# Kernel optimization log

Hardware: AMD Instinct MI355X
Metric: run time of the kernel (lower is better)

The kernel has to match this reference:

```python
import jax, jax.numpy as jnp
import numpy as np

B, SQ, SK = 8, 128, 128
IVD, DIM, EV, H, NH = 32, 32, 64, 8, 128
DK = EV // H


def setup_inputs() -> dict:
    key = jax.random.key(0)
    ks = jax.random.split(key, 16)
    n = lambda k, s: jax.random.normal(k, s, dtype=jnp.float32)
    lin = lambda k, fi, fo: n(k, (fi, fo)) / np.float32(np.sqrt(fi))
    d = {}
    d['query_value'] = n(ks[0], (B, SQ, IVD))
    d['key_value']   = n(ks[1], (B, SK, IVD))
    d['value']       = n(ks[2], (B, SK, DIM))
    d['impute_data'] = n(ks[3], (B, SQ, IVD // 2))
    d['emb_mask'] = jax.random.randint(ks[4], (B, SK, DIM), 0, 2).astype(jnp.int32)
    # learn_value_embedding: Linear(IVD,NH)+Tanh+Linear(NH,EV,no bias)
    d['w1'] = lin(ks[5], IVD, NH); d['b1'] = jnp.zeros((NH,), jnp.float32)
    d['w2'] = lin(ks[6], NH, EV)
    # linears[0], linears[1]: Linear(EV,EV)
    d['wq'] = lin(ks[7], EV, EV); d['bq'] = jnp.zeros((EV,), jnp.float32)
    d['wk'] = lin(ks[8], EV, EV); d['bk'] = jnp.zeros((EV,), jnp.float32)
    # linears[2]: Linear(DIM*H, NH)
    d['wo'] = lin(ks[9], DIM * H, NH); d['bo'] = jnp.zeros((NH,), jnp.float32)
    # query_data_enc: Linear(IVD/2,NH)+LayerNorm(NH)+ReLU+Linear(NH,NH)
    d['wd1'] = lin(ks[10], IVD // 2, NH); d['bd1'] = jnp.zeros((NH,), jnp.float32)
    d['ln_g'] = jnp.ones((NH,), jnp.float32); d['ln_b'] = jnp.zeros((NH,), jnp.float32)
    d['wd2'] = lin(ks[11], NH, NH); d['bd2'] = jnp.zeros((NH,), jnp.float32)
    return d


def reference(query_value, key_value, value, impute_data,
              w1, b1, w2, wq, bq, wk, bk, wo, bo,
              wd1, bd1, ln_g, ln_b, wd2, bd2, emb_mask):
    b = query_value.shape[0]
    dim = value.shape[-1]
    # value embeddings: Linear -> Tanh -> Linear(no bias)
    qe = jnp.tanh(query_value @ w1 + b1) @ w2   # [B,Sq,EV]
    ke = jnp.tanh(key_value @ w1 + b1) @ w2     # [B,Sk,EV]
    q = (qe @ wq + bq).reshape(b, -1, H, DK).transpose(0, 2, 1, 3)  # [B,H,Sq,DK]
    k = (ke @ wk + bk).reshape(b, -1, H, DK).transpose(0, 2, 1, 3)  # [B,H,Sk,DK]
    scores = jnp.einsum('bhqd,bhkd->bhqk', q, k) / np.float32(np.sqrt(DK))
    # broadcast scores over the value channel dim; masked_fill with -10000
    m = emb_mask[:, None, None, :, :]           # [B,1,1,Sk,dim]
    logits = jnp.where(m == 0, jnp.float32(-10000.0), scores[..., None])  # [B,H,Sq,Sk,dim]
    p_attn = jax.nn.softmax(logits, axis=-2)    # softmax over Sk per channel
    out = jnp.einsum('bhqkd,bkd->bhqd', p_attn, value)  # [B,H,Sq,dim]
    x = out.transpose(0, 2, 1, 3).reshape(b, -1, H * dim)
    y = x @ wo + bo                             # [B,Sq,NH]
    # query_data_enc branch
    h1 = impute_data @ wd1 + bd1
    mu = jnp.mean(h1, axis=-1, keepdims=True)
    var = jnp.var(h1, axis=-1, keepdims=True)
    ln = (h1 - mu) / jnp.sqrt(var + 1e-5) * ln_g + ln_b
    query_data = jax.nn.relu(ln) @ wd2 + bd2    # [B,Sq,NH]
    return y, query_data
```

## Files before the change

### kernel.cpp

```cpp
#include <hip/hip_runtime.h>
#include <math.h>

#define B 8
#define SQ 128
#define SK 128
#define IVD 32
#define DIM 32
#define EV 64
#define H 8
#define NH 128
#define DK 8

__global__ __launch_bounds__(128) void proj_kernel(
    const float* __restrict__ qv, const float* __restrict__ kv,
    const float* __restrict__ w1, const float* __restrict__ b1,
    const float* __restrict__ w2,
    const float* __restrict__ wq, const float* __restrict__ bq,
    const float* __restrict__ wk, const float* __restrict__ bk,
    float* __restrict__ qout, float* __restrict__ kout)
{
    const int r = blockIdx.x;
    const int tid = threadIdx.x;
    const float* src; const float* wp; const float* bp; float* dst;
    if (r < B * SQ) {
        src = qv + r * IVD; wp = wq; bp = bq; dst = qout + r * EV;
    } else {
        int rr = r - B * SQ;
        src = kv + rr * IVD; wp = wk; bp = bk; dst = kout + rr * EV;
    }
    __shared__ float xs[IVD];
    __shared__ float h1[NH];
    __shared__ float ev[EV];
    if (tid < IVD) xs[tid] = src[tid];
    __syncthreads();
    float acc = b1[tid];
    #pragma unroll
    for (int i = 0; i < IVD; ++i) acc += xs[i] * w1[i * NH + tid];
    h1[tid] = tanhf(acc);
    __syncthreads();
    if (tid < EV) {
        float a = 0.f;
        #pragma unroll 8
        for (int i = 0; i < NH; ++i) a += h1[i] * w2[i * EV + tid];
        ev[tid] = a;
    }
    __syncthreads();
    if (tid < EV) {
        float a = bp[tid];
        #pragma unroll 8
        for (int j = 0; j < EV; ++j) a += ev[j] * wp[j * EV + tid];
        dst[tid] = a;
    }
}

__global__ __launch_bounds__(256) void attn_kernel(
    const float* __restrict__ qproj, const float* __restrict__ kproj,
    const float* __restrict__ value, const int* __restrict__ mask,
    const float* __restrict__ wo, const float* __restrict__ bo,
    float* __restrict__ y)
{
    const int bq = blockIdx.x;
    const int b = bq >> 7;
    const int tid = threadIdx.x;

    __shared__ float qs[EV];
    __shared__ float sc[H * SK];
    __shared__ float hmax[H];
    __shared__ float vm[SK * DIM];
    __shared__ float mm[SK * DIM];
    __shared__ float xr[H * DIM];
    __shared__ float ypart[256];

    if (tid < EV) qs[tid] = qproj[bq * EV + tid];
    for (int idx = tid; idx < SK * DIM; idx += 256) {
        vm[idx] = value[b * SK * DIM + idx];
        mm[idx] = (float)mask[b * SK * DIM + idx];
    }
    __syncthreads();

    for (int p = tid; p < H * SK; p += 256) {
        const int h = p >> 7, k = p & 127;
        const float* kr = kproj + (b * SK + k) * EV + h * DK;
        float d = 0.f;
        #pragma unroll
        for (int j = 0; j < DK; ++j) d += qs[h * DK + j] * kr[j];
        sc[p] = d * 0.3535533905932738f;
    }
    __syncthreads();

    if (tid < H) {
        float m = -1e30f;
        for (int k = 0; k < SK; ++k) m = fmaxf(m, sc[tid * SK + k]);
        hmax[tid] = m;
    }
    __syncthreads();
    for (int p = tid; p < H * SK; p += 256) {
        const int h = p >> 7;
        sc[p] = __expf(sc[p] - hmax[h]);
    }
    __syncthreads();

    {
        const int h = tid >> 5, d = tid & 31;
        float num = 0.f, den = 0.f;
        #pragma unroll 4
        for (int k = 0; k < SK; ++k) {
            const float w = sc[h * SK + k] * mm[k * DIM + d];
            num += w * vm[k * DIM + d];
            den += w;
        }
        xr[tid] = num / den;
    }
    __syncthreads();

    {
        const int n = tid & 127, half = tid >> 7;
        const float* wop = wo + half * 128 * NH;
        const float* xp = xr + half * 128;
        float a = 0.f;
        #pragma unroll 8
        for (int j = 0; j < 128; ++j) a += xp[j] * wop[j * NH + n];
        ypart[tid] = a;
    }
    __syncthreads();
    if (tid < NH) {
        y[bq * NH + tid] = ypart[tid] + ypart[tid + 128] + bo[tid];
    }
}

__global__ __launch_bounds__(128) void impute_kernel(
    const float* __restrict__ imp,
    const float* __restrict__ wd1, const float* __restrict__ bd1,
    const float* __restrict__ ln_g, const float* __restrict__ ln_b,
    const float* __restrict__ wd2, const float* __restrict__ bd2,
    float* __restrict__ out)
{
    const int bs = blockIdx.x;
    const int tid = threadIdx.x;
    __shared__ float xs[IVD / 2];
    __shared__ float h1[NH];
    __shared__ float red[2];

    if (tid < IVD / 2) xs[tid] = imp[bs * (IVD / 2) + tid];
    __syncthreads();
    float acc = bd1[tid];
    #pragma unroll
    for (int i = 0; i < IVD / 2; ++i) acc += xs[i] * wd1[i * NH + tid];

    float s = acc;
    #pragma unroll
    for (int off = 32; off > 0; off >>= 1) s += __shfl_down(s, off, 64);
    if ((tid & 63) == 0) red[tid >> 6] = s;
    __syncthreads();
    const float mean = (red[0] + red[1]) * (1.f / NH);
    const float diff = acc - mean;
    float s2 = diff * diff;
    __syncthreads();
    #pragma unroll
    for (int off = 32; off > 0; off >>= 1) s2 += __shfl_down(s2, off, 64);
    if ((tid & 63) == 0) red[tid >> 6] = s2;
    __syncthreads();
    const float var = (red[0] + red[1]) * (1.f / NH);

    const float ln = diff * rsqrtf(var + 1e-5f) * ln_g[tid] + ln_b[tid];
    h1[tid] = fmaxf(ln, 0.f);
    __syncthreads();

    float a = bd2[tid];
    #pragma unroll 8
    for (int j = 0; j < NH; ++j) a += h1[j] * wd2[j * NH + tid];
    out[bs * NH + tid] = a;
}

extern "C" void kernel_launch(void* const* d_in, const int* in_sizes, int n_in,
                              void* d_out, int out_size, void* d_ws, size_t ws_size,
                              hipStream_t stream) {
    const float* query_value = (const float*)d_in[0];
    const float* key_value   = (const float*)d_in[1];
    const float* value       = (const float*)d_in[2];
    const float* impute      = (const float*)d_in[3];
    const int*   emb_mask    = (const int*)d_in[4];
    const float* w1   = (const float*)d_in[5];
    const float* b1   = (const float*)d_in[6];
    const float* w2   = (const float*)d_in[7];
    const float* wq   = (const float*)d_in[8];
    const float* bq   = (const float*)d_in[9];
    const float* wk   = (const float*)d_in[10];
    const float* bk   = (const float*)d_in[11];
    const float* wo   = (const float*)d_in[12];
    const float* bo   = (const float*)d_in[13];
    const float* wd1  = (const float*)d_in[14];
    const float* bd1  = (const float*)d_in[15];
    const float* ln_g = (const float*)d_in[16];
    const float* ln_b = (const float*)d_in[17];
    const float* wd2  = (const float*)d_in[18];
    const float* bd2  = (const float*)d_in[19];

    float* y  = (float*)d_out;
    float* qd = y + B * SQ * NH;

    float* qproj = (float*)d_ws;
    float* kproj = qproj + B * SQ * EV;

    hipLaunchKernelGGL(proj_kernel, dim3(B * (SQ + SK)), dim3(128), 0, stream,
                       query_value, key_value, w1, b1, w2, wq, bq, wk, bk, qproj, kproj);
    hipLaunchKernelGGL(attn_kernel, dim3(B * SQ), dim3(256), 0, stream,
                       qproj, kproj, value, emb_mask, wo, bo, y);
    hipLaunchKernelGGL(impute_kernel, dim3(B * SQ), dim3(128), 0, stream,
                       impute, wd1, bd1, ln_g, ln_b, wd2, bd2, qd);
}
```

Before: 127.6 us.

## Fuse impute into projection kernel and process two queries per attention block

```diff
diff --git a/kernel.cpp b/kernel.cpp
--- a/kernel.cpp
+++ b/kernel.cpp
@@ -10,46 +10,100 @@
 #define H 8
 #define NH 128
 #define DK 8
-
-__global__ __launch_bounds__(128) void proj_kernel(
+#define TQ 2
+#define PAD 132
+
+__global__ __launch_bounds__(128) void fused1_kernel(
     const float* __restrict__ qv, const float* __restrict__ kv,
     const float* __restrict__ w1, const float* __restrict__ b1,
     const float* __restrict__ w2,
-    const float* __restrict__ wq, const float* __restrict__ bq,
-    const float* __restrict__ wk, const float* __restrict__ bk,
-    float* __restrict__ qout, float* __restrict__ kout)
+    const float* __restrict__ wq, const float* __restrict__ bqv,
+    const float* __restrict__ wk, const float* __restrict__ bkv,
+    float* __restrict__ qout, float* __restrict__ kout,
+    const float* __restrict__ imp,
+    const float* __restrict__ wd1, const float* __restrict__ bd1,
+    const float* __restrict__ ln_g, const float* __restrict__ ln_b,
+    const float* __restrict__ wd2, const float* __restrict__ bd2,
+    float* __restrict__ qd)
 {
     const int r = blockIdx.x;
     const int tid = threadIdx.x;
-    const float* src; const float* wp; const float* bp; float* dst;
-    if (r < B * SQ) {
-        src = qv + r * IVD; wp = wq; bp = bq; dst = qout + r * EV;
+
+    if (r < 2 * B * SQ) {
+        __shared__ float xs[IVD];
+        __shared__ float h1[NH];
+        __shared__ float ev[EV];
+        __shared__ float part[128];
+        const float* src; const float* wp; const float* bp; float* dst;
+        if (r < B * SQ) {
+            src = qv + r * IVD; wp = wq; bp = bqv; dst = qout + r * EV;
+        } else {
+            const int rr = r - B * SQ;
+            src = kv + rr * IVD; wp = wk; bp = bkv; dst = kout + rr * EV;
+        }
+        if (tid < IVD) xs[tid] = src[tid];
+        __syncthreads();
+        float acc = b1[tid];
+        #pragma unroll
+        for (int i = 0; i < IVD; ++i) acc += xs[i] * w1[i * NH + tid];
+        h1[tid] = tanhf(acc);
+        __syncthreads();
+
+        const int o = tid & 63, hf = tid >> 6;
+        {
+            float a = 0.f;
+            const float* w2p = w2 + o;
+            #pragma unroll 8
+            for (int i = hf * 64; i < hf * 64 + 64; ++i) a += h1[i] * w2p[i * EV];
+            part[tid] = a;
+        }
+        __syncthreads();
+        if (tid < EV) ev[tid] = part[tid] + part[tid + 64];
+        __syncthreads();
+        {
+            float a = 0.f;
+            const float* wpp = wp + o;
+            #pragma unroll 8
+            for (int j = hf * 32; j < hf * 32 + 32; ++j) a += ev[j] * wpp[j * EV];
+            part[tid] = a;
+        }
+        __syncthreads();
+        if (tid < EV) dst[tid] = part[tid] + part[tid + 64] + bp[tid];
     } else {
-        int rr = r - B * SQ;
-        src = kv + rr * IVD; wp = wk; bp = bk; dst = kout + rr * EV;
-    }
-    __shared__ float xs[IVD];
-    __shared__ float h1[NH];
-    __shared__ float ev[EV];
-    if (tid < IVD) xs[tid] = src[tid];
-    __syncthreads();
-    float acc = b1[tid];
-    #pragma unroll
-    for (int i = 0; i < IVD; ++i) acc += xs[i] * w1[i * NH + tid];
-    h1[tid] = tanhf(acc);
-    __syncthreads();
-    if (tid < EV) {
-        float a = 0.f;
+        const int bs = r - 2 * B * SQ;
+        __shared__ float xs2[IVD / 2];
+        __shared__ float h1b[NH];
+        __shared__ float red[2];
+
+        if (tid < IVD / 2) xs2[tid] = imp[bs * (IVD / 2) + tid];
+        __syncthreads();
+        float acc = bd1[tid];
+        #pragma unroll
+        for (int i = 0; i < IVD / 2; ++i) acc += xs2[i] * wd1[i * NH + tid];
+
+        float s = acc;
+        #pragma unroll
+        for (int off = 32; off > 0; off >>= 1) s += __shfl_down(s, off, 64);
+        if ((tid & 63) == 0) red[tid >> 6] = s;
+        __syncthreads();
+        const float mean = (red[0] + red[1]) * (1.f / NH);
+        const float diff = acc - mean;
+        float s2 = diff * diff;
+        __syncthreads();
+        #pragma unroll
+        for (int off = 32; off > 0; off >>= 1) s2 += __shfl_down(s2, off, 64);
+        if ((tid & 63) == 0) red[tid >> 6] = s2;
+        __syncthreads();
+        const float var = (red[0] + red[1]) * (1.f / NH);
+
+        const float ln = diff * rsqrtf(var + 1e-5f) * ln_g[tid] + ln_b[tid];
+        h1b[tid] = fmaxf(ln, 0.f);
+        __syncthreads();
+
+        float a = bd2[tid];
         #pragma unroll 8
-        for (int i = 0; i < NH; ++i) a += h1[i] * w2[i * EV + tid];
-        ev[tid] = a;
-    }
-    __syncthreads();
-    if (tid < EV) {
-        float a = bp[tid];
-        #pragma unroll 8
-        for (int j = 0; j < EV; ++j) a += ev[j] * wp[j * EV + tid];
-        dst[tid] = a;
+        for (int j = 0; j < NH; ++j) a += h1b[j] * wd2[j * NH + tid];
+        qd[bs * NH + tid] = a;
     }
 }
 
@@ -59,117 +113,103 @@
     const float* __restrict__ wo, const float* __restrict__ bo,
     float* __restrict__ y)
 {
-    const int bq = blockIdx.x;
-    const int b = bq >> 7;
+    const int blk = blockIdx.x;
+    const int b = blk >> 6;
+    const int q0 = (blk & 63) * TQ;
     const int tid = threadIdx.x;
 
-    __shared__ float qs[EV];
-    __shared__ float sc[H * SK];
-    __shared__ float hmax[H];
-    __shared__ float vm[SK * DIM];
-    __shared__ float mm[SK * DIM];
-    __shared__ float xr[H * DIM];
-    __shared__ float ypart[256];
-
-    if (tid < EV) qs[tid] = qproj[bq * EV + tid];
+    __shared__ __align__(16) float qs[TQ * EV];
+    __shared__ __align__(16) float sc[TQ * H * SK];
+    __shared__ __align__(16) float mvt[DIM * PAD];
+    __shared__ __align__(16) float mmt[DIM * PAD];
+    __shared__ __align__(16) float xr[TQ * H * DIM];
+    __shared__ __align__(16) float ypart[2 * TQ * NH];
+    __shared__ float hmax[TQ * H];
+
+    if (tid < TQ * EV) qs[tid] = qproj[(b * SQ + q0) * EV + tid];
     for (int idx = tid; idx < SK * DIM; idx += 256) {
-        vm[idx] = value[b * SK * DIM + idx];
-        mm[idx] = (float)mask[b * SK * DIM + idx];
-    }
-    __syncthreads();
-
-    for (int p = tid; p < H * SK; p += 256) {
-        const int h = p >> 7, k = p & 127;
+        const int k = idx >> 5, d = idx & 31;
+        const float v = value[b * SK * DIM + idx];
+        const float m = (float)mask[b * SK * DIM + idx];
+        mvt[d * PAD + k] = v * m;
+        mmt[d * PAD + k] = m;
+    }
+    __syncthreads();
+
+    #pragma unroll
+    for (int i = 0; i < (TQ * H * SK) / 256; ++i) {
+        const int p = tid + i * 256;
+        const int q = p >> 10, rem = p & 1023, h = rem >> 7, k = rem & 127;
         const float* kr = kproj + (b * SK + k) * EV + h * DK;
-        float d = 0.f;
-        #pragma unroll
-        for (int j = 0; j < DK; ++j) d += qs[h * DK + j] * kr[j];
-        sc[p] = d * 0.3535533905932738f;
-    }
-    __syncthreads();
-
-    if (tid < H) {
+        const float* qq = qs + q * EV + h * DK;
+        float dsum = 0.f;
+        #pragma unroll
+        for (int j = 0; j < DK; ++j) dsum += qq[j] * kr[j];
+        sc[p] = dsum * 0.3535533905932738f;
+    }
+    __syncthreads();
+
+    {
+        const int grp = tid >> 4, ln = tid & 15;
         float m = -1e30f;
-        for (int k = 0; k < SK; ++k) m = fmaxf(m, sc[tid * SK + k]);
-        hmax[tid] = m;
-    }
-    __syncthreads();
-    for (int p = tid; p < H * SK; p += 256) {
-        const int h = p >> 7;
-        sc[p] = __expf(sc[p] - hmax[h]);
+        #pragma unroll
+        for (int j = 0; j < 8; ++j) m = fmaxf(m, sc[(grp << 7) + ln * 8 + j]);
+        #pragma unroll
+        for (int off = 8; off; off >>= 1) m = fmaxf(m, __shfl_down(m, off, 16));
+        if (ln == 0) hmax[grp] = m;
+    }
+    __syncthreads();
+    {
+        const int grp = tid >> 4, ln = tid & 15;
+        const float hm = hmax[grp];
+        #pragma unroll
+        for (int j = 0; j < 8; ++j) {
+            const int idx = (grp << 7) + ln * 8 + j;
+            sc[idx] = __expf(sc[idx] - hm);
+        }
     }
     __syncthreads();
 
     {
         const int h = tid >> 5, d = tid & 31;
-        float num = 0.f, den = 0.f;
+        const float4* vp = (const float4*)&mvt[d * PAD];
+        const float4* mp = (const float4*)&mmt[d * PAD];
+        #pragma unroll
+        for (int q = 0; q < TQ; ++q) {
+            const float4* sp = (const float4*)&sc[(q * H + h) * SK];
+            float num = 0.f, den = 0.f;
+            #pragma unroll 8
+            for (int k4 = 0; k4 < SK / 4; ++k4) {
+                const float4 s = sp[k4], v = vp[k4], m = mp[k4];
+                num += s.x * v.x + s.y * v.y + s.z * v.z + s.w * v.w;
+                den += s.x * m.x + s.y * m.y + s.z * m.z + s.w * m.w;
+            }
+            xr[q * (H * DIM) + h * DIM + d] = num / den;
+        }
+    }
+    __syncthreads();
+
+    {
+        const int n = tid & 127, half = tid >> 7;
+        const float* wop = wo + half * 128 * NH + n;
+        const float* x0 = xr + half * 128;
+        const float* x1 = xr + (H * DIM) + half * 128;
+        float a0 = 0.f, a1 = 0.f;
         #pragma unroll 4
-        for (int k = 0; k < SK; ++k) {
-            const float w = sc[h * SK + k] * mm[k * DIM + d];
-            num += w * vm[k * DIM + d];
-            den += w;
-        }
-        xr[tid] = num / den;
-    }
-    __syncthreads();
-
-    {
-        const int n = tid & 127, half = tid >> 7;
-        const float* wop = wo + half * 128 * NH;
-        const float* xp = xr + half * 128;
-        float a = 0.f;
-        #pragma unroll 8
-        for (int j = 0; j < 128; ++j) a += xp[j] * wop[j * NH + n];
-        ypart[tid] = a;
-    }
-    __syncthreads();
-    if (tid < NH) {
-        y[bq * NH + tid] = ypart[tid] + ypart[tid + 128] + bo[tid];
-    }
-}
-
-__global__ __launch_bounds__(128) void impute_kernel(
-    const float* __restrict__ imp,
-    const float* __restrict__ wd1, const float* __restrict__ bd1,
-    const float* __restrict__ ln_g, const float* __restrict__ ln_b,
-    const float* __restrict__ wd2, const float* __restrict__ bd2,
-    float* __restrict__ out)
-{
-    const int bs = blockIdx.x;
-    const int tid = threadIdx.x;
-    __shared__ float xs[IVD / 2];
-    __shared__ float h1[NH];
-    __shared__ float red[2];
-
-    if (tid < IVD / 2) xs[tid] = imp[bs * (IVD / 2) + tid];
-    __syncthreads();
-    float acc = bd1[tid];
-    #pragma unroll
-    for (int i = 0; i < IVD / 2; ++i) acc += xs[i] * wd1[i * NH + tid];
-
-    float s = acc;
-    #pragma unroll
-    for (int off = 32; off > 0; off >>= 1) s += __shfl_down(s, off, 64);
-    if ((tid & 63) == 0) red[tid >> 6] = s;
-    __syncthreads();
-    const float mean = (red[0] + red[1]) * (1.f / NH);
-    const float diff = acc - mean;
-    float s2 = diff * diff;
-    __syncthreads();
-    #pragma unroll
-    for (int off = 32; off > 0; off >>= 1) s2 += __shfl_down(s2, off, 64);
-    if ((tid & 63) == 0) red[tid >> 6] = s2;
-    __syncthreads();
-    const float var = (red[0] + red[1]) * (1.f / NH);
-
-    const float ln = diff * rsqrtf(var + 1e-5f) * ln_g[tid] + ln_b[tid];
-    h1[tid] = fmaxf(ln, 0.f);
-    __syncthreads();
-
-    float a = bd2[tid];
-    #pragma unroll 8
-    for (int j = 0; j < NH; ++j) a += h1[j] * wd2[j * NH + tid];
-    out[bs * NH + tid] = a;
+        for (int j = 0; j < 128; ++j) {
+            const float w = wop[j * NH];
+            a0 += w * x0[j];
+            a1 += w * x1[j];
+        }
+        ypart[half * (TQ * NH) + 0 * NH + n] = a0;
+        ypart[half * (TQ * NH) + 1 * NH + n] = a1;
+    }
+    __syncthreads();
+    {
+        const int q = tid >> 7, n = tid & 127;
+        y[(b * SQ + q0 + q) * NH + n] =
+            ypart[q * NH + n] + ypart[TQ * NH + q * NH + n] + bo[n];
+    }
 }
 
 extern "C" void kernel_launch(void* const* d_in, const int* in_sizes, int n_in,
@@ -202,10 +242,10 @@
     float* qproj = (float*)d_ws;
     float* kproj = qproj + B * SQ * EV;
 
-    hipLaunchKernelGGL(proj_kernel, dim3(B * (SQ + SK)), dim3(128), 0, stream,
-                       query_value, key_value, w1, b1, w2, wq, bq, wk, bk, qproj, kproj);
-    hipLaunchKernelGGL(attn_kernel, dim3(B * SQ), dim3(256), 0, stream,
+    hipLaunchKernelGGL(fused1_kernel, dim3(3 * B * SQ), dim3(128), 0, stream,
+                       query_value, key_value, w1, b1, w2, wq, bq, wk, bk,
+                       qproj, kproj,
+                       impute, wd1, bd1, ln_g, ln_b, wd2, bd2, qd);
+    hipLaunchKernelGGL(attn_kernel, dim3(B * SQ / TQ), dim3(256), 0, stream,
                        qproj, kproj, value, emb_mask, wo, bo, y);
-    hipLaunchKernelGGL(impute_kernel, dim3(B * SQ), dim3(128), 0, stream,
-                       impute, wd1, bd1, ln_g, ln_b, wd2, bd2, qd);
 }
```

Result: faster. 117.3 us (-8.1%).
